# Kernel tuning notes

Measured on AMD Instinct MI355X. Metric: run time of the kernel, lower is better.

Reference implementation:

```python
import jax, jax.numpy as jnp
import numpy as np

N_V, M, K, C, H, F, CO = 100000, 25000, 48, 64, 4, 256, 64


def setup_inputs() -> dict:
    key = jax.random.key(0)
    ks = jax.random.split(key, 16)
    w = lambda k, shape: (jax.random.normal(k, shape, jnp.float32) * 0.05)
    voxel_features = jax.random.normal(ks[0], (N_V, C), jnp.float32)
    voxel_coords = jax.random.uniform(ks[1], (N_V, 3), jnp.float32) * 70.0 - 35.0
    query_coords = jax.random.uniform(ks[2], (M, 3), jnp.float32) * 70.0 - 35.0
    key_indices = jax.random.randint(ks[3], (M, K), 0, N_V, jnp.int32)
    key_mask = jax.random.uniform(ks[4], (M, K)) < 0.3
    key_mask = key_mask.at[:, 0].set(False)  # guarantee >=1 valid key per query
    zeros = lambda n: jnp.zeros((n,), jnp.float32)
    ones = lambda n: jnp.ones((n,), jnp.float32)
    return dict(
        voxel_features=voxel_features, voxel_coords=voxel_coords,
        query_coords=query_coords, key_indices=key_indices, key_mask=key_mask,
        q_pos_w=w(ks[5], (C, 3)), q_pos_b=zeros(C),
        k_pos_w=w(ks[6], (C, 3)), k_pos_b=zeros(C),
        in_proj_w=w(ks[7], (3 * C, C)), in_proj_b=zeros(3 * C),
        out_proj_w=w(ks[8], (C, C)), out_proj_b=zeros(C),
        lin1_w=w(ks[9], (F, C)), lin1_b=zeros(F),
        lin2_w=w(ks[10], (C, F)), lin2_b=zeros(C),
        norm_g=ones(C), norm_b=zeros(C), norm_m=zeros(C), norm_v=ones(C),
        out_w=w(ks[11], (CO, C)), out_b=zeros(CO),
        bn2_g=ones(CO), bn2_b=zeros(CO), bn2_m=zeros(CO), bn2_v=ones(CO),
    )


def reference(voxel_features, voxel_coords, query_coords, key_indices, key_mask,
              q_pos_w, q_pos_b, k_pos_w, k_pos_b, in_proj_w, in_proj_b,
              out_proj_w, out_proj_b, lin1_w, lin1_b, lin2_w, lin2_b,
              norm_g, norm_b, norm_m, norm_v, out_w, out_b,
              bn2_g, bn2_b, bn2_m, bn2_v):
    m, k = key_indices.shape
    c = voxel_features.shape[1]
    h = H
    d = c // h
    # grouping_operation: gather per-query key features/coords  (M,K,C)/(M,K,3)
    key_feats = voxel_features[key_indices]
    rel = voxel_coords[key_indices] - query_coords[:, None, :]  # relative coords
    # k_pos_proj: Conv1d(3->C, kernel 1) + ReLU == pointwise linear
    key_pos = jax.nn.relu(jnp.einsum('mkt,ct->mkc', rel, k_pos_w) + k_pos_b)
    k_in = key_feats + key_pos                      # (M,K,C)
    # q_pos_proj: Linear(3->C) + ReLU
    q_in = jax.nn.relu(query_coords @ q_pos_w.T + q_pos_b)  # (M,C)
    # nn.MultiheadAttention, query len 1, batch = M, keys = K
    wq, wk, wv = jnp.split(in_proj_w, 3, axis=0)
    bq, bk, bv = jnp.split(in_proj_b, 3)
    q = ((q_in @ wq.T + bq) * (d ** -0.5)).reshape(m, h, d)
    kk = (k_in @ wk.T + bk).reshape(m, k, h, d)
    vv = (k_in @ wv.T + bv).reshape(m, k, h, d)
    s = jnp.einsum('mhd,mkhd->mhk', q, kk)
    s = jnp.where(key_mask[:, None, :], -1e9, s)    # key_padding_mask
    a = jax.nn.softmax(s, axis=-1)
    o = jnp.einsum('mhk,mkhd->mhd', a, vv).reshape(m, c)
    attend = o @ out_proj_w.T + out_proj_b          # (M,C)
    # FFN residual (dropouts are identity in eval)
    ff = jax.nn.relu(attend @ lin1_w.T + lin1_b) @ lin2_w.T + lin2_b
    x = attend + ff
    # BatchNorm1d (eval)
    x = (x - norm_m) / jnp.sqrt(norm_v + 1e-5) * norm_g + norm_b
    # output_layer: Linear -> BN -> ReLU
    y = x @ out_w.T + out_b
    y = (y - bn2_m) / jnp.sqrt(bn2_v + 1e-5) * bn2_g + bn2_b
    return jax.nn.relu(y)
```

## Files before the change

kernel.cpp:

```cpp
#include <hip/hip_runtime.h>
#include <math.h>

#define CC 64
#define KK 48
#define HH 4

typedef __attribute__((ext_vector_type(8))) short s16x8;
typedef __attribute__((ext_vector_type(4))) short s16x4;
typedef __attribute__((ext_vector_type(4))) float f32x4;

#define QW_OFF_U16 57344
#define CASTB 1024

#define WAVEFENCE() asm volatile("s_waitcnt lgkmcnt(0)" ::: "memory")

__device__ __forceinline__ unsigned short f2bf(float f) {
  return (unsigned short)((__float_as_uint(f) + 0x8000u) >> 16);
}
__device__ __forceinline__ float bf2f(unsigned short h) {
  return __uint_as_float(((unsigned)h) << 16);
}

__global__ __launch_bounds__(256) void setup_kernel(
    const float* __restrict__ ipw, const float* __restrict__ opw,
    const float* __restrict__ l1w, const float* __restrict__ l2w,
    const float* __restrict__ ow,
    const float* __restrict__ ng, const float* __restrict__ nb,
    const float* __restrict__ nm, const float* __restrict__ nv,
    const float* __restrict__ b2g, const float* __restrict__ b2b,
    const float* __restrict__ b2m, const float* __restrict__ b2v,
    const unsigned char* __restrict__ km,
    const float* __restrict__ vf, const float* __restrict__ vcoord,
    const float* __restrict__ qcoord, const float* __restrict__ qpw,
    const float* __restrict__ qpb, const float* __restrict__ ipb,
    float* __restrict__ ws,
    unsigned short* __restrict__ vfb, float4* __restrict__ vc4,
    unsigned short* __restrict__ qw_out, int M, int NV)
{
  unsigned short* wsu = (unsigned short*)ws;
  const int b = blockIdx.x;

  if (b < 210) {
    if (b == 209) {
      int any = 0;
      for (int i = threadIdx.x; i < 4096; i += 256)
        if ((i & 3) && km[i]) any = 1;
      __shared__ int sb;
      if (threadIdx.x == 0) sb = 0;
      __syncthreads();
      if (any) atomicOr(&sb, 1);
      __syncthreads();
      if (threadIdx.x == 0) ((int*)ws)[26880] = sb;
      return;
    }
    int e = b * 256 + threadIdx.x;
    if (e < 4096)        wsu[e] = f2bf(ipw[e]);
    else if (e < 8192)  { int i = e - 4096; int h = i >> 10, c = (i >> 4) & 63, d = i & 15;
                          wsu[e] = f2bf(ipw[(size_t)(64 + h * 16 + d) * 64 + c]); }
    else if (e < 12288)  wsu[e] = f2bf(ipw[e]);
    else if (e < 16384)  wsu[e] = f2bf(opw[e - 12288]);
    else if (e < 32768)  wsu[e] = f2bf(l1w[e - 16384]);
    else if (e < 49152)  wsu[e] = f2bf(l2w[e - 32768]);
    else if (e < 53248)  wsu[e] = f2bf(ow[e - 49152]);
    else if (e < 53312) { int c = e - 53248; float s = ng[c] / sqrtf(nv[c] + 1e-5f);
                          ws[26624 + c] = s; ws[26624 + 64 + c] = nb[c] - nm[c] * s; }
    else if (e < 53376) { int c = e - 53312; float s = b2g[c] / sqrtf(b2v[c] + 1e-5f);
                          ws[26752 + c] = s; ws[26752 + 64 + c] = b2b[c] - b2m[c] * s; }
    return;
  }

  if (b < 210 + CASTB) {
    const int i0 = (b - 210) * 256 + threadIdx.x;
    const int stride = CASTB * 256;
    for (int i = i0; i < NV * 16; i += stride) {
      const float4 v = *(const float4*)(vf + (size_t)i * 4);
      s16x4 p; p[0] = (short)f2bf(v.x); p[1] = (short)f2bf(v.y);
      p[2] = (short)f2bf(v.z); p[3] = (short)f2bf(v.w);
      *(s16x4*)(vfb + (size_t)i * 4) = p;
    }
    for (int i = i0; i < NV; i += stride)
      vc4[i] = make_float4(vcoord[i * 3], vcoord[i * 3 + 1], vcoord[i * 3 + 2], 0.f);
    return;
  }

  {
    __shared__ __align__(16) unsigned short wql[4096];
    __shared__ __align__(16) unsigned short wkTl[4096];
    __shared__ __align__(16) unsigned short xa[4][1024];
    __shared__ float qc[4][48];
    const int w = threadIdx.x >> 6, l = threadIdx.x & 63;
    const int col = l & 15, lg = l >> 4;
    const int r0 = (b - 210 - CASTB) * 64 + w * 16;

    for (int i = threadIdx.x; i < 4096; i += 256) {
      const int r = i >> 6, d = i & 63;
      wql[i ^ ((r & 7) << 3)] = f2bf(ipw[i]);
      wkTl[(d * 64 + r) ^ ((d & 7) << 3)] = f2bf(ipw[4096 + i]);
    }
    if (l < 48) {
      int gi = r0 * 3 + l;
      qc[w][l] = (gi < M * 3) ? qcoord[gi] : 0.f;
    }
    const int c0 = col * 4;
    const float4 wA = *(const float4*)(qpw + c0 * 3);
    const float4 wB = *(const float4*)(qpw + c0 * 3 + 4);
    const float4 wC = *(const float4*)(qpw + c0 * 3 + 8);
    const float4 bq4 = *(const float4*)(qpb + c0);
    __syncthreads();

    #pragma unroll
    for (int i = 0; i < 4; ++i) {
      const int row = i * 4 + lg;
      const float x = qc[w][row * 3 + 0], y = qc[w][row * 3 + 1], z = qc[w][row * 3 + 2];
      s16x4 p;
      p[0] = (short)f2bf(fmaxf(wA.x * x + wA.y * y + wA.z * z + bq4.x, 0.f));
      p[1] = (short)f2bf(fmaxf(wA.w * x + wB.x * y + wB.y * z + bq4.y, 0.f));
      p[2] = (short)f2bf(fmaxf(wB.z * x + wB.w * y + wC.x * z + bq4.z, 0.f));
      p[3] = (short)f2bf(fmaxf(wC.y * x + wC.z * y + wC.w * z + bq4.w, 0.f));
      *(s16x4*)&xa[w][(row * 64 + c0) ^ ((row & 7) << 3)] = p;
    }
    __syncthreads();

    {
      s16x8 af0 = *(const s16x8*)&xa[w][(col * 64 + 0 + lg * 8) ^ ((col & 7) << 3)];
      s16x8 af1 = *(const s16x8*)&xa[w][(col * 64 + 32 + lg * 8) ^ ((col & 7) << 3)];
      f32x4 qv[4];
      #pragma unroll
      for (int nt = 0; nt < 4; ++nt) {
        const int n = nt * 16 + col;
        f32x4 acc = {0.f, 0.f, 0.f, 0.f};
        acc = __builtin_amdgcn_mfma_f32_16x16x32_bf16(af0,
                *(const s16x8*)&wql[(n * 64 + 0 + lg * 8) ^ ((col & 7) << 3)], acc, 0, 0, 0);
        acc = __builtin_amdgcn_mfma_f32_16x16x32_bf16(af1,
                *(const s16x8*)&wql[(n * 64 + 32 + lg * 8) ^ ((col & 7) << 3)], acc, 0, 0, 0);
        qv[nt] = acc;
      }
      __syncthreads();
      #pragma unroll
      for (int nt = 0; nt < 4; ++nt) {
        const int n = nt * 16 + col;
        const float bb = ipb[n];
        #pragma unroll
        for (int r = 0; r < 4; ++r) {
          const int row = lg * 4 + r;
          xa[w][(row * 64 + n) ^ ((row & 7) << 3)] = f2bf((qv[nt][r] + bb) * 0.25f);
        }
      }
    }
    __syncthreads();

    #pragma unroll
    for (int h = 0; h < HH; ++h) {
      s16x8 a = {0, 0, 0, 0, 0, 0, 0, 0};
      if (lg < 2)
        a = *(const s16x8*)&xa[w][(col * 64 + h * 16 + lg * 8) ^ ((col & 7) << 3)];
      #pragma unroll
      for (int nt = 0; nt < 4; ++nt) {
        const int n = nt * 16 + col;
        s16x8 bf = {0, 0, 0, 0, 0, 0, 0, 0};
        if (lg < 2)
          bf = *(const s16x8*)&wkTl[(n * 64 + h * 16 + lg * 8) ^ ((col & 7) << 3)];
        f32x4 acc = {0.f, 0.f, 0.f, 0.f};
        acc = __builtin_amdgcn_mfma_f32_16x16x32_bf16(a, bf, acc, 0, 0, 0);
        #pragma unroll
        for (int r = 0; r < 4; ++r) {
          const int m = lg * 4 + r;
          if (r0 + m < M)
            qw_out[(size_t)(r0 + m) * 256 + h * 64 + n] = f2bf(acc[r]);
        }
      }
    }
  }
}

__global__ __launch_bounds__(256, 4) void attn_hot(
    const unsigned short* __restrict__ vfb, const float4* __restrict__ vc4,
    const float* __restrict__ qcoord, const int* __restrict__ kidx,
    const unsigned char* __restrict__ km8, const int* __restrict__ km32,
    const int* __restrict__ maskfmt,
    const float* __restrict__ kpw, const float* __restrict__ kpb,
    const float* __restrict__ ipb,
    const unsigned short* __restrict__ wv_bf,
    const unsigned short* __restrict__ qw_pre,
    float* __restrict__ out, int M)
{
  __shared__ __align__(16) unsigned short shq[4][3456];
  const int w = threadIdx.x >> 6, l = threadIdx.x & 63;
  const int col = l & 15, lg = l >> 4;
  int m = blockIdx.x * 4 + w;
  if (m >= M) m = M - 1;
  unsigned short* sh = shq[w];
  float* relf = (float*)(sh + 3072);
  const int is_u8 = *maskfmt;

  s16x8 wvb[4][2];
  #pragma unroll
  for (int nt = 0; nt < 4; ++nt)
    #pragma unroll
    for (int kst = 0; kst < 2; ++kst)
      wvb[nt][kst] = *(const s16x8*)(wv_bf + (size_t)(nt * 16 + col) * 64 + kst * 32 + lg * 8);

  const float qx = qcoord[m * 3 + 0], qy = qcoord[m * 3 + 1], qz = qcoord[m * 3 + 2];
  const int c0 = col * 4;
  const float4 kwA = *(const float4*)(kpw + c0 * 3);
  const float4 kwB = *(const float4*)(kpw + c0 * 3 + 4);
  const float4 kwC = *(const float4*)(kpw + c0 * 3 + 8);
  const float4 kbv = *(const float4*)(kpb + c0);

  const s16x8 qb0 = *(const s16x8*)(qw_pre + (size_t)m * 256 + (col & 3) * 64 + 0 + lg * 8);
  const s16x8 qb1 = *(const s16x8*)(qw_pre + (size_t)m * 256 + (col & 3) * 64 + 32 + lg * 8);

  unsigned char msk = 0;
  if (l < KK) {
    const int idx = kidx[m * KK + l];
    msk = is_u8 ? km8[m * KK + l] : (unsigned char)(km32[m * KK + l] != 0);
    const float4 vc = vc4[idx];
    float4 rr;
    rr.x = vc.x - qx; rr.y = vc.y - qy; rr.z = vc.z - qz;
    rr.w = __int_as_float(idx);
    *(float4*)(relf + l * 4) = rr;
  }
  const unsigned long long bm = __ballot(l < KK && msk);
  WAVEFENCE();

  #pragma unroll
  for (int half = 0; half < 2; ++half) {
    float4 ra[6]; s16x4 va[6];
    #pragma unroll
    for (int j = 0; j < 6; ++j) {
      const int k = half * 24 + j * 4 + lg;
      ra[j] = *(const float4*)(relf + k * 4);
      va[j] = *(const s16x4*)(vfb + (size_t)__float_as_int(ra[j].w) * 64 + c0);
    }
    #pragma unroll
    for (int j = 0; j < 6; ++j) {
      const int k = half * 24 + j * 4 + lg;
      const float p0 = fmaxf(kwA.x * ra[j].x + kwA.y * ra[j].y + kwA.z * ra[j].z + kbv.x, 0.f);
      const float p1 = fmaxf(kwA.w * ra[j].x + kwB.x * ra[j].y + kwB.y * ra[j].z + kbv.y, 0.f);
      const float p2 = fmaxf(kwB.z * ra[j].x + kwB.w * ra[j].y + kwC.x * ra[j].z + kbv.z, 0.f);
      const float p3 = fmaxf(kwC.y * ra[j].x + kwC.z * ra[j].y + kwC.w * ra[j].z + kbv.w, 0.f);
      s16x4 p;
      p[0] = (short)f2bf(bf2f((unsigned short)va[j][0]) + p0);
      p[1] = (short)f2bf(bf2f((unsigned short)va[j][1]) + p1);
      p[2] = (short)f2bf(bf2f((unsigned short)va[j][2]) + p2);
      p[3] = (short)f2bf(bf2f((unsigned short)va[j][3]) + p3);
      *(s16x4*)&sh[(k * 64 + c0) ^ ((k & 7) << 3)] = p;
    }
  }
  WAVEFENCE();

  s16x8 af[3][2];
  #pragma unroll
  for (int mt = 0; mt < 3; ++mt)
    #pragma unroll
    for (int kst = 0; kst < 2; ++kst) {
      const int row = mt * 16 + col;
      af[mt][kst] = *(const s16x8*)&sh[(row * 64 + kst * 32 + lg * 8) ^ ((row & 7) << 3)];
    }
  f32x4 sc[3];
  sc[0] = sc[1] = sc[2] = (f32x4){0.f, 0.f, 0.f, 0.f};
  __builtin_amdgcn_s_setprio(1);
  #pragma unroll
  for (int mt = 0; mt < 3; ++mt) {
    sc[mt] = __builtin_amdgcn_mfma_f32_16x16x32_bf16(af[mt][0], qb0, sc[mt], 0, 0, 0);
    sc[mt] = __builtin_amdgcn_mfma_f32_16x16x32_bf16(af[mt][1], qb1, sc[mt], 0, 0, 0);
  }
  __builtin_amdgcn_s_setprio(0);

  float sv[12];
  {
    float mx = -INFINITY;
    #pragma unroll
    for (int mt = 0; mt < 3; ++mt)
      #pragma unroll
      for (int r = 0; r < 4; ++r) {
        const int key = mt * 16 + lg * 4 + r;
        float v = sc[mt][r];
        if ((bm >> key) & 1ull) v = -1e30f;
        sv[mt * 4 + r] = v;
        mx = fmaxf(mx, v);
      }
    mx = fmaxf(mx, __shfl_xor(mx, 16, 64));
    mx = fmaxf(mx, __shfl_xor(mx, 32, 64));
    float sum = 0.f;
    #pragma unroll
    for (int i = 0; i < 12; ++i) { float e = __expf(sv[i] - mx); sv[i] = e; sum += e; }
    sum += __shfl_xor(sum, 16, 64);
    sum += __shfl_xor(sum, 32, 64);
    const float inv = 1.f / sum;
    #pragma unroll
    for (int i = 0; i < 12; ++i) sv[i] *= inv;
  }
  if (col < HH) {
    #pragma unroll
    for (int mt = 0; mt < 3; ++mt)
      #pragma unroll
      for (int r = 0; r < 4; ++r)
        relf[(mt * 16 + lg * 4 + r) * 4 + col] = sv[mt * 4 + r];
  }
  WAVEFENCE();

  f32x4 vva[4][3];
  __builtin_amdgcn_s_setprio(1);
  #pragma unroll
  for (int nt = 0; nt < 4; ++nt) {
    vva[nt][0] = vva[nt][1] = vva[nt][2] = (f32x4){0.f, 0.f, 0.f, 0.f};
    #pragma unroll
    for (int kst = 0; kst < 2; ++kst) {
      vva[nt][0] = __builtin_amdgcn_mfma_f32_16x16x32_bf16(af[0][kst], wvb[nt][kst], vva[nt][0], 0, 0, 0);
      vva[nt][1] = __builtin_amdgcn_mfma_f32_16x16x32_bf16(af[1][kst], wvb[nt][kst], vva[nt][1], 0, 0, 0);
      vva[nt][2] = __builtin_amdgcn_mfma_f32_16x16x32_bf16(af[2][kst], wvb[nt][kst], vva[nt][2], 0, 0, 0);
    }
  }
  __builtin_amdgcn_s_setprio(0);
  float op[4] = {0.f, 0.f, 0.f, 0.f};
  #pragma unroll
  for (int mt = 0; mt < 3; ++mt)
    #pragma unroll
    for (int r = 0; r < 4; ++r) {
      const float4 a4 = *(const float4*)(relf + (mt * 16 + lg * 4 + r) * 4);
      op[0] += a4.x * vva[0][mt][r];
      op[1] += a4.y * vva[1][mt][r];
      op[2] += a4.z * vva[2][mt][r];
      op[3] += a4.w * vva[3][mt][r];
    }
  #pragma unroll
  for (int nt = 0; nt < 4; ++nt) {
    op[nt] += __shfl_xor(op[nt], 16, 64);
    op[nt] += __shfl_xor(op[nt], 32, 64);
  }
  {
    float oo = (lg == 0) ? op[0] : (lg == 1) ? op[1] : (lg == 2) ? op[2] : op[3];
    oo += ipb[2 * CC + lg * 16 + col];
    out[(size_t)m * CC + lg * 16 + col] = oo;
  }
}

__global__ __launch_bounds__(256) void prep_kernel(
    const float* __restrict__ ipw, const float* __restrict__ opw,
    const float* __restrict__ l1w, const float* __restrict__ l2w,
    const float* __restrict__ ow,
    const float* __restrict__ ng, const float* __restrict__ nb,
    const float* __restrict__ nm, const float* __restrict__ nv,
    const float* __restrict__ b2g, const float* __restrict__ b2b,
    const float* __restrict__ b2m, const float* __restrict__ b2v,
    const unsigned char* __restrict__ km,
    float* __restrict__ ws)
{
  unsigned short* wsu = (unsigned short*)ws;
  if (blockIdx.x == 209) {
    int any = 0;
    for (int i = threadIdx.x; i < 4096; i += 256)
      if ((i & 3) && km[i]) any = 1;
    __shared__ int sb;
    if (threadIdx.x == 0) sb = 0;
    __syncthreads();
    if (any) atomicOr(&sb, 1);
    __syncthreads();
    if (threadIdx.x == 0) ((int*)ws)[26880] = sb;
    return;
  }
  int e = blockIdx.x * 256 + threadIdx.x;
  if (e < 4096)        wsu[e] = f2bf(ipw[e]);
  else if (e < 8192)  { int i = e - 4096; int h = i >> 10, c = (i >> 4) & 63, d = i & 15;
                        wsu[e] = f2bf(ipw[(size_t)(64 + h * 16 + d) * 64 + c]); }
  else if (e < 12288)  wsu[e] = f2bf(ipw[e]);
  else if (e < 16384)  wsu[e] = f2bf(opw[e - 12288]);
  else if (e < 32768)  wsu[e] = f2bf(l1w[e - 16384]);
  else if (e < 49152)  wsu[e] = f2bf(l2w[e - 32768]);
  else if (e < 53248)  wsu[e] = f2bf(ow[e - 49152]);
  else if (e < 53312) { int c = e - 53248; float s = ng[c] / sqrtf(nv[c] + 1e-5f);
                        ws[26624 + c] = s; ws[26624 + 64 + c] = nb[c] - nm[c] * s; }
  else if (e < 53376) { int c = e - 53312; float s = b2g[c] / sqrtf(b2v[c] + 1e-5f);
                        ws[26752 + c] = s; ws[26752 + 64 + c] = b2b[c] - b2m[c] * s; }
}

__global__ __launch_bounds__(256, 4) void attn_fallback(
    const float* __restrict__ vfeat, const float* __restrict__ vcoord,
    const float* __restrict__ qcoord, const int* __restrict__ kidx,
    const unsigned char* __restrict__ km8, const int* __restrict__ km32,
    const int* __restrict__ maskfmt,
    const float* __restrict__ qpw, const float* __restrict__ qpb,
    const float* __restrict__ kpw, const float* __restrict__ kpb,
    const float* __restrict__ ipb,
    const unsigned short* __restrict__ wq_bf,
    const unsigned short* __restrict__ wk2T_bf,
    const unsigned short* __restrict__ wv_bf,
    float* __restrict__ out, int M)
{
  __shared__ __align__(16) unsigned short shq[4][3776];
  __shared__ __align__(16) unsigned short wvl[4096];
  const int w = threadIdx.x >> 6, l = threadIdx.x & 63;
  const int col = l & 15, lg = l >> 4;
  int m = blockIdx.x * 4 + w;
  if (m >= M) m = M - 1;
  unsigned short* sh = shq[w];
  const int is_u8 = *maskfmt;
  float* relf = (float*)sh + 1696;

  #pragma unroll
  for (int i = 0; i < 2; ++i) {
    const int ch = threadIdx.x * 2 + i;
    const int n = ch >> 3, g = ch & 7;
    const s16x8 v = *(const s16x8*)(wv_bf + n * 64 + g * 8);
    *(s16x8*)&wvl[n * 64 + ((g ^ (n & 7)) << 3)] = v;
  }

  const float qx = qcoord[m * 3 + 0], qy = qcoord[m * 3 + 1], qz = qcoord[m * 3 + 2];
  const int c0 = col * 4;
  const float4 kwA = *(const float4*)(kpw + c0 * 3);
  const float4 kwB = *(const float4*)(kpw + c0 * 3 + 4);
  const float4 kwC = *(const float4*)(kpw + c0 * 3 + 8);
  const float4 kbv = *(const float4*)(kpb + c0);

  {
    float v = qpw[l * 3 + 0] * qx + qpw[l * 3 + 1] * qy + qpw[l * 3 + 2] * qz + qpb[l];
    sh[3328 + l] = f2bf(fmaxf(v, 0.f));
  }
  unsigned char msk = 0;
  if (l < KK) {
    int idx = kidx[m * KK + l];
    msk = is_u8 ? km8[m * KK + l] : (unsigned char)(km32[m * KK + l] != 0);
    relf[l * 4 + 0] = vcoord[idx * 3 + 0] - qx;
    relf[l * 4 + 1] = vcoord[idx * 3 + 1] - qy;
    relf[l * 4 + 2] = vcoord[idx * 3 + 2] - qz;
    relf[l * 4 + 3] = __int_as_float(idx);
  }
  const unsigned long long bm = __ballot(l < KK && msk);
  __syncthreads();

  {
    f32x4 qacc[4];
    #pragma unroll
    for (int nt = 0; nt < 4; ++nt) qacc[nt] = (f32x4){0.f, 0.f, 0.f, 0.f};
    #pragma unroll
    for (int kst = 0; kst < 2; ++kst) {
      const s16x8 a = *(const s16x8*)&sh[3328 + kst * 32 + lg * 8];
      #pragma unroll
      for (int nt = 0; nt < 4; ++nt) {
        const s16x8 b = *(const s16x8*)(wq_bf + (nt * 16 + col) * 64 + kst * 32 + lg * 8);
        qacc[nt] = __builtin_amdgcn_mfma_f32_16x16x32_bf16(a, b, qacc[nt], 0, 0, 0);
      }
    }
    __syncthreads();
    if (lg == 0) {
      #pragma unroll
      for (int nt = 0; nt < 4; ++nt)
        sh[3328 + nt * 16 + col] = f2bf((qacc[nt][0] + ipb[nt * 16 + col]) * 0.25f);
    }
    __syncthreads();
    f32x4 wacc[4];
    #pragma unroll
    for (int nt = 0; nt < 4; ++nt) wacc[nt] = (f32x4){0.f, 0.f, 0.f, 0.f};
    #pragma unroll
    for (int kst = 0; kst < 2; ++kst) {
      const int hblk = kst * 2 + (lg >> 1);
      s16x8 a = {0, 0, 0, 0, 0, 0, 0, 0};
      if (col == hblk) a = *(const s16x8*)&sh[3328 + kst * 32 + lg * 8];
      #pragma unroll
      for (int nt = 0; nt < 4; ++nt) {
        const s16x8 b = *(const s16x8*)(wk2T_bf + hblk * 1024 + (nt * 16 + col) * 16 + (lg & 1) * 8);
        wacc[nt] = __builtin_amdgcn_mfma_f32_16x16x32_bf16(a, b, wacc[nt], 0, 0, 0);
      }
    }
    if (lg == 0) {
      #pragma unroll
      for (int nt = 0; nt < 4; ++nt)
        #pragma unroll
        for (int r = 0; r < 4; ++r)
          sh[3072 + r * 64 + nt * 16 + col] = f2bf(wacc[nt][r]);
    }
  }

  #pragma unroll
  for (int half = 0; half < 2; ++half) {
    float4 ra[6], va[6];
    #pragma unroll
    for (int j = 0; j < 6; ++j) {
      const int k = half * 24 + j * 4 + lg;
      ra[j] = *(const float4*)(relf + k * 4);
      va[j] = *(const float4*)(vfeat + (size_t)__float_as_int(ra[j].w) * 64 + c0);
    }
    #pragma unroll
    for (int j = 0; j < 6; ++j) {
      const int k = half * 24 + j * 4 + lg;
      const float p0 = fmaxf(kwA.x * ra[j].x + kwA.y * ra[j].y + kwA.z * ra[j].z + kbv.x, 0.f);
      const float p1 = fmaxf(kwA.w * ra[j].x + kwB.x * ra[j].y + kwB.y * ra[j].z + kbv.y, 0.f);
      const float p2 = fmaxf(kwB.z * ra[j].x + kwB.w * ra[j].y + kwC.x * ra[j].z + kbv.z, 0.f);
      const float p3 = fmaxf(kwC.y * ra[j].x + kwC.z * ra[j].y + kwC.w * ra[j].z + kbv.w, 0.f);
      s16x4 p;
      p[0] = (short)f2bf(va[j].x + p0); p[1] = (short)f2bf(va[j].y + p1);
      p[2] = (short)f2bf(va[j].z + p2); p[3] = (short)f2bf(va[j].w + p3);
      *(s16x4*)&sh[(k * 64 + c0) ^ ((k & 7) << 3)] = p;
    }
  }
  __syncthreads();

  s16x8 af[3][2];
  #pragma unroll
  for (int mt = 0; mt < 3; ++mt)
    #pragma unroll
    for (int kst = 0; kst < 2; ++kst) {
      const int row = mt * 16 + col;
      af[mt][kst] = *(const s16x8*)&sh[(row * 64 + kst * 32 + lg * 8) ^ ((row & 7) << 3)];
    }
  f32x4 sc[3];
  sc[0] = sc[1] = sc[2] = (f32x4){0.f, 0.f, 0.f, 0.f};
  #pragma unroll
  for (int kst = 0; kst < 2; ++kst) {
    const s16x8 b = *(const s16x8*)&sh[3072 + (col & 3) * 64 + kst * 32 + lg * 8];
    #pragma unroll
    for (int mt = 0; mt < 3; ++mt)
      sc[mt] = __builtin_amdgcn_mfma_f32_16x16x32_bf16(af[mt][kst], b, sc[mt], 0, 0, 0);
  }

  float sv[12];
  {
    float mx = -INFINITY;
    #pragma unroll
    for (int mt = 0; mt < 3; ++mt)
      #pragma unroll
      for (int r = 0; r < 4; ++r) {
        const int key = mt * 16 + lg * 4 + r;
        float v = sc[mt][r];
        if ((bm >> key) & 1ull) v = -1e30f;
        sv[mt * 4 + r] = v;
        mx = fmaxf(mx, v);
      }
    mx = fmaxf(mx, __shfl_xor(mx, 16, 64));
    mx = fmaxf(mx, __shfl_xor(mx, 32, 64));
    float sum = 0.f;
    #pragma unroll
    for (int i = 0; i < 12; ++i) { float e = __expf(sv[i] - mx); sv[i] = e; sum += e; }
    sum += __shfl_xor(sum, 16, 64);
    sum += __shfl_xor(sum, 32, 64);
    const float inv = 1.f / sum;
    #pragma unroll
    for (int i = 0; i < 12; ++i) sv[i] *= inv;
  }

  float op[4];
  #pragma unroll
  for (int nt = 0; nt < 4; ++nt) {
    const int n = nt * 16 + col;
    f32x4 vv0 = {0.f, 0.f, 0.f, 0.f}, vv1 = vv0, vv2 = vv0;
    #pragma unroll
    for (int kst = 0; kst < 2; ++kst) {
      const s16x8 b = *(const s16x8*)&wvl[(n * 64 + kst * 32 + lg * 8) ^ ((n & 7) << 3)];
      vv0 = __builtin_amdgcn_mfma_f32_16x16x32_bf16(af[0][kst], b, vv0, 0, 0, 0);
      vv1 = __builtin_amdgcn_mfma_f32_16x16x32_bf16(af[1][kst], b, vv1, 0, 0, 0);
      vv2 = __builtin_amdgcn_mfma_f32_16x16x32_bf16(af[2][kst], b, vv2, 0, 0, 0);
    }
    const int src = lg * 16 + nt;
    float o = 0.f;
    #pragma unroll
    for (int mt = 0; mt < 3; ++mt)
      #pragma unroll
      for (int r = 0; r < 4; ++r) {
        const float a = __shfl(sv[mt * 4 + r], src, 64);
        const float v = (mt == 0) ? vv0[r] : (mt == 1) ? vv1[r] : vv2[r];
        o += a * v;
      }
    op[nt] = o;
  }
  #pragma unroll
  for (int nt = 0; nt < 4; ++nt) {
    op[nt] += __shfl_xor(op[nt], 16, 64);
    op[nt] += __shfl_xor(op[nt], 32, 64);
  }
  {
    float oo = (lg == 0) ? op[0] : (lg == 1) ? op[1] : (lg == 2) ? op[2] : op[3];
    oo += ipb[2 * CC + lg * 16 + col];
    out[(size_t)m * CC + lg * 16 + col] = oo;
  }
}

__global__ __launch_bounds__(256, 2) void chain_kernel(
    float* __restrict__ inout, const unsigned short* __restrict__ wsu,
    const float* __restrict__ opb, const float* __restrict__ l1b,
    const float* __restrict__ l2b, const float* __restrict__ ob,
    const float* __restrict__ nrm, const float* __restrict__ bn2, int M)
{
  __shared__ short lds[4][5120];
  const int w = threadIdx.x >> 6;
  const int l = threadIdx.x & 63;
  const int col = l & 15, lg = l >> 4;
  const int r0 = blockIdx.x * 64 + w * 16;

  short* XH = &lds[w][0];
  short* XB = &lds[w][4096];
  const unsigned short* opw_bf = wsu + 12288;
  const unsigned short* l1_bf  = wsu + 16384;
  const unsigned short* l2_bf  = wsu + 32768;
  const unsigned short* ow_bf  = wsu + 49152;

  #pragma unroll
  for (int i = 0; i < 4; ++i) {
    int row = i * 4 + lg, cb = col * 4;
    float4 v = make_float4(0.f, 0.f, 0.f, 0.f);
    if (r0 + row < M) v = *(const float4*)(&inout[(size_t)(r0 + row) * 64 + cb]);
    s16x4 p; p[0] = (short)f2bf(v.x); p[1] = (short)f2bf(v.y);
    p[2] = (short)f2bf(v.z); p[3] = (short)f2bf(v.w);
    *(s16x4*)&XH[(row * 64 + cb) ^ ((row & 7) << 3)] = p;
  }

  s16x8 afa[2];
  #pragma unroll
  for (int kst = 0; kst < 2; ++kst)
    afa[kst] = *(const s16x8*)&XH[(col * 64 + kst * 32 + lg * 8) ^ ((col & 7) << 3)];
  f32x4 att[4];
  #pragma unroll
  for (int nt = 0; nt < 4; ++nt) {
    f32x4 acc = {0.f, 0.f, 0.f, 0.f};
    #pragma unroll
    for (int kst = 0; kst < 2; ++kst) {
      const s16x8 b = *(const s16x8*)&opw_bf[(nt * 16 + col) * 64 + kst * 32 + lg * 8];
      acc = __builtin_amdgcn_mfma_f32_16x16x32_bf16(afa[kst], b, acc, 0, 0, 0);
    }
    float bias = opb[nt * 16 + col];
    #pragma unroll
    for (int r = 0; r < 4; ++r) {
      acc[r] += bias;
      int row = lg * 4 + r;
      XB[(row * 64 + nt * 16 + col) ^ ((row & 7) << 3)] = (short)f2bf(acc[r]);
    }
    att[nt] = acc;
  }

  s16x8 afb[2];
  #pragma unroll
  for (int kst = 0; kst < 2; ++kst)
    afb[kst] = *(const s16x8*)&XB[(col * 64 + kst * 32 + lg * 8) ^ ((col & 7) << 3)];
  #pragma unroll
  for (int nt = 0; nt < 16; ++nt) {
    f32x4 acc = {0.f, 0.f, 0.f, 0.f};
    #pragma unroll
    for (int kst = 0; kst < 2; ++kst) {
      const s16x8 b = *(const s16x8*)&l1_bf[(nt * 16 + col) * 64 + kst * 32 + lg * 8];
      acc = __builtin_amdgcn_mfma_f32_16x16x32_bf16(afb[kst], b, acc, 0, 0, 0);
    }
    float bias = l1b[nt * 16 + col];
    #pragma unroll
    for (int r = 0; r < 4; ++r) {
      float h = fmaxf(acc[r] + bias, 0.f);
      int row = lg * 4 + r;
      XH[(row * 256 + nt * 16 + col) ^ ((row & 7) << 3)] = (short)f2bf(h);
    }
  }

  s16x8 afh[8];
  #pragma unroll
  for (int kst = 0; kst < 8; ++kst)
    afh[kst] = *(const s16x8*)&XH[(col * 256 + kst * 32 + lg * 8) ^ ((col & 7) << 3)];
  #pragma unroll
  for (int nt = 0; nt < 4; ++nt) {
    f32x4 acc = {0.f, 0.f, 0.f, 0.f};
    #pragma unroll
    for (int kst = 0; kst < 8; ++kst) {
      const s16x8 b = *(const s16x8*)&l2_bf[(nt * 16 + col) * 256 + kst * 32 + lg * 8];
      acc = __builtin_amdgcn_mfma_f32_16x16x32_bf16(afh[kst], b, acc, 0, 0, 0);
    }
    int nc = nt * 16 + col;
    float bias = l2b[nc], sN = nrm[nc], tN = nrm[64 + nc];
    #pragma unroll
    for (int r = 0; r < 4; ++r) {
      float x = (att[nt][r] + acc[r] + bias) * sN + tN;
      int row = lg * 4 + r;
      XB[(row * 64 + nc) ^ ((row & 7) << 3)] = (short)f2bf(x);
    }
  }

  s16x8 afx[2];
  #pragma unroll
  for (int kst = 0; kst < 2; ++kst)
    afx[kst] = *(const s16x8*)&XB[(col * 64 + kst * 32 + lg * 8) ^ ((col & 7) << 3)];
  #pragma unroll
  for (int nt = 0; nt < 4; ++nt) {
    f32x4 acc = {0.f, 0.f, 0.f, 0.f};
    #pragma unroll
    for (int kst = 0; kst < 2; ++kst) {
      const s16x8 b = *(const s16x8*)&ow_bf[(nt * 16 + col) * 64 + kst * 32 + lg * 8];
      acc = __builtin_amdgcn_mfma_f32_16x16x32_bf16(afx[kst], b, acc, 0, 0, 0);
    }
    int nc = nt * 16 + col;
    float bias = ob[nc], sB = bn2[nc], tB = bn2[64 + nc];
    #pragma unroll
    for (int r = 0; r < 4; ++r) {
      float y = fmaxf((acc[r] + bias) * sB + tB, 0.f);
      int row = lg * 4 + r;
      if (r0 + row < M) inout[(size_t)(r0 + row) * 64 + nc] = y;
    }
  }
}

extern "C" void kernel_launch(void* const* d_in, const int* in_sizes, int n_in,
                              void* d_out, int out_size, void* d_ws, size_t ws_size,
                              hipStream_t stream) {
  const float* vfeat  = (const float*)d_in[0];
  const float* vcoord = (const float*)d_in[1];
  const float* qcoord = (const float*)d_in[2];
  const int*   kidx   = (const int*)d_in[3];
  const unsigned char* km8  = (const unsigned char*)d_in[4];
  const int*           km32 = (const int*)d_in[4];
  const float* qpw = (const float*)d_in[5];
  const float* qpb = (const float*)d_in[6];
  const float* kpw = (const float*)d_in[7];
  const float* kpb = (const float*)d_in[8];
  const float* ipw = (const float*)d_in[9];
  const float* ipb = (const float*)d_in[10];
  const float* opw = (const float*)d_in[11];
  const float* opb = (const float*)d_in[12];
  const float* l1w = (const float*)d_in[13];
  const float* l1b = (const float*)d_in[14];
  const float* l2w = (const float*)d_in[15];
  const float* l2b = (const float*)d_in[16];
  const float* ng  = (const float*)d_in[17];
  const float* nb  = (const float*)d_in[18];
  const float* nm  = (const float*)d_in[19];
  const float* nv  = (const float*)d_in[20];
  const float* ow  = (const float*)d_in[21];
  const float* ob  = (const float*)d_in[22];
  const float* b2g = (const float*)d_in[23];
  const float* b2b = (const float*)d_in[24];
  const float* b2m = (const float*)d_in[25];
  const float* b2v = (const float*)d_in[26];

  const int M  = in_sizes[2] / 3;
  const int NV = in_sizes[0] / 64;
  float* ws  = (float*)d_ws;
  float* out = (float*)d_out;
  unsigned short* wsu = (unsigned short*)ws;
  const int* flag = (const int*)ws + 26880;

  const size_t need = (size_t)114688 + (size_t)M * 512 + (size_t)NV * 128 + (size_t)NV * 16;
  const int hot = (ws_size >= need) ? 1 : 0;
  unsigned short* qw  = wsu + QW_OFF_U16;
  unsigned short* vfb = wsu + QW_OFF_U16 + (size_t)M * 256;
  float4* vc4 = (float4*)(wsu + QW_OFF_U16 + (size_t)M * 256 + (size_t)NV * 64);

  if (hot) {
    const int qblocks = (M + 63) / 64;
    setup_kernel<<<210 + CASTB + qblocks, 256, 0, stream>>>(
        ipw, opw, l1w, l2w, ow, ng, nb, nm, nv, b2g, b2b, b2m, b2v, km8,
        vfeat, vcoord, qcoord, qpw, qpb, ipb, ws, vfb, vc4, qw, M, NV);
    attn_hot<<<(M + 3) / 4, 256, 0, stream>>>(vfb, vc4, qcoord, kidx,
                                              km8, km32, flag, kpw, kpb, ipb,
                                              wsu + 8192, qw, out, M);
  } else {
    prep_kernel<<<210, 256, 0, stream>>>(ipw, opw, l1w, l2w, ow,
                                         ng, nb, nm, nv, b2g, b2b, b2m, b2v, km8, ws);
    attn_fallback<<<(M + 3) / 4, 256, 0, stream>>>(vfeat, vcoord, qcoord, kidx,
                                                   km8, km32, flag,
                                                   qpw, qpb, kpw, kpb, ipb,
                                                   wsu, wsu + 4096, wsu + 8192, out, M);
  }
  chain_kernel<<<(M + 63) / 64, 256, 0, stream>>>(out, wsu, opb, l1b, l2b, ob,
                                                  ws + 26624, ws + 26752, M);
}
```

Measured before the change: 95.91 us.

## Split FFN chain across waves per 16-row tile and stage Wv in LDS

The post-attention chain kernel now gives each 256-thread block 16 rows instead of 64. Its four waves split the output columns of each GEMM and exchange activations through shared LDS with block barriers, which launches four times as many blocks with less per-wave register and LDS pressure. The attention kernel also loads the Wv bf16 weights cooperatively into a swizzled LDS buffer instead of holding eight weight vectors per lane in registers, with the wave fence replaced by a block barrier. The intent is higher occupancy and lower register use. The cost is extra block-wide syncs, more redundant weight fetches per row, and LDS reads on the MFMA path.

```diff
diff --git a/kernel.cpp b/kernel.cpp
--- a/kernel.cpp
+++ b/kernel.cpp
@@ -185,6 +185,7 @@
     float* __restrict__ out, int M)
 {
   __shared__ __align__(16) unsigned short shq[4][3456];
+  __shared__ __align__(16) unsigned short wvl[4096];
   const int w = threadIdx.x >> 6, l = threadIdx.x & 63;
   const int col = l & 15, lg = l >> 4;
   int m = blockIdx.x * 4 + w;
@@ -193,12 +194,13 @@
   float* relf = (float*)(sh + 3072);
   const int is_u8 = *maskfmt;
 
-  s16x8 wvb[4][2];
-  #pragma unroll
-  for (int nt = 0; nt < 4; ++nt)
-    #pragma unroll
-    for (int kst = 0; kst < 2; ++kst)
-      wvb[nt][kst] = *(const s16x8*)(wv_bf + (size_t)(nt * 16 + col) * 64 + kst * 32 + lg * 8);
+  #pragma unroll
+  for (int i = 0; i < 2; ++i) {
+    const int ch = threadIdx.x * 2 + i;
+    const int n = ch >> 3, g = ch & 7;
+    const s16x8 v = *(const s16x8*)(wv_bf + n * 64 + g * 8);
+    *(s16x8*)&wvl[n * 64 + ((g ^ (n & 7)) << 3)] = v;
+  }
 
   const float qx = qcoord[m * 3 + 0], qy = qcoord[m * 3 + 1], qz = qcoord[m * 3 + 2];
   const int c0 = col * 4;
@@ -221,7 +223,7 @@
     *(float4*)(relf + l * 4) = rr;
   }
   const unsigned long long bm = __ballot(l < KK && msk);
-  WAVEFENCE();
+  __syncthreads();
 
   #pragma unroll
   for (int half = 0; half < 2; ++half) {
@@ -304,12 +306,14 @@
   __builtin_amdgcn_s_setprio(1);
   #pragma unroll
   for (int nt = 0; nt < 4; ++nt) {
+    const int n = nt * 16 + col;
     vva[nt][0] = vva[nt][1] = vva[nt][2] = (f32x4){0.f, 0.f, 0.f, 0.f};
     #pragma unroll
     for (int kst = 0; kst < 2; ++kst) {
-      vva[nt][0] = __builtin_amdgcn_mfma_f32_16x16x32_bf16(af[0][kst], wvb[nt][kst], vva[nt][0], 0, 0, 0);
-      vva[nt][1] = __builtin_amdgcn_mfma_f32_16x16x32_bf16(af[1][kst], wvb[nt][kst], vva[nt][1], 0, 0, 0);
-      vva[nt][2] = __builtin_amdgcn_mfma_f32_16x16x32_bf16(af[2][kst], wvb[nt][kst], vva[nt][2], 0, 0, 0);
+      const s16x8 bb = *(const s16x8*)&wvl[(n * 64 + kst * 32 + lg * 8) ^ ((n & 7) << 3)];
+      vva[nt][0] = __builtin_amdgcn_mfma_f32_16x16x32_bf16(af[0][kst], bb, vva[nt][0], 0, 0, 0);
+      vva[nt][1] = __builtin_amdgcn_mfma_f32_16x16x32_bf16(af[1][kst], bb, vva[nt][1], 0, 0, 0);
+      vva[nt][2] = __builtin_amdgcn_mfma_f32_16x16x32_bf16(af[2][kst], bb, vva[nt][2], 0, 0, 0);
     }
   }
   __builtin_amdgcn_s_setprio(0);
@@ -333,6 +337,128 @@
     float oo = (lg == 0) ? op[0] : (lg == 1) ? op[1] : (lg == 2) ? op[2] : op[3];
     oo += ipb[2 * CC + lg * 16 + col];
     out[(size_t)m * CC + lg * 16 + col] = oo;
+  }
+}
+
+__global__ __launch_bounds__(256, 4) void chain2_kernel(
+    float* __restrict__ inout, const unsigned short* __restrict__ wsu,
+    const float* __restrict__ opb, const float* __restrict__ l1b,
+    const float* __restrict__ l2b, const float* __restrict__ ob,
+    const float* __restrict__ nrm, const float* __restrict__ bn2, int M)
+{
+  __shared__ __align__(16) unsigned short XA[1024];
+  __shared__ __align__(16) unsigned short XH[4096];
+  __shared__ __align__(16) unsigned short XB[1024];
+  const int w = threadIdx.x >> 6, l = threadIdx.x & 63;
+  const int col = l & 15, lg = l >> 4;
+  const int r0 = blockIdx.x * 16;
+
+  const unsigned short* opw_bf = wsu + 12288;
+  const unsigned short* l1_bf  = wsu + 16384;
+  const unsigned short* l2_bf  = wsu + 32768;
+  const unsigned short* ow_bf  = wsu + 49152;
+
+  {
+    const int i = threadIdx.x;
+    const int row = i >> 4, cb = (i & 15) * 4;
+    float4 v = make_float4(0.f, 0.f, 0.f, 0.f);
+    if (r0 + row < M) v = *(const float4*)(&inout[(size_t)(r0 + row) * 64 + cb]);
+    s16x4 p; p[0] = (short)f2bf(v.x); p[1] = (short)f2bf(v.y);
+    p[2] = (short)f2bf(v.z); p[3] = (short)f2bf(v.w);
+    *(s16x4*)&XA[(row * 64 + cb) ^ ((row & 7) << 3)] = p;
+  }
+  __syncthreads();
+
+  s16x8 afa[2];
+  #pragma unroll
+  for (int kst = 0; kst < 2; ++kst)
+    afa[kst] = *(const s16x8*)&XA[(col * 64 + kst * 32 + lg * 8) ^ ((col & 7) << 3)];
+  f32x4 att;
+  {
+    f32x4 acc = {0.f, 0.f, 0.f, 0.f};
+    #pragma unroll
+    for (int kst = 0; kst < 2; ++kst) {
+      const s16x8 bb = *(const s16x8*)&opw_bf[(w * 16 + col) * 64 + kst * 32 + lg * 8];
+      acc = __builtin_amdgcn_mfma_f32_16x16x32_bf16(afa[kst], bb, acc, 0, 0, 0);
+    }
+    const float bias = opb[w * 16 + col];
+    #pragma unroll
+    for (int r = 0; r < 4; ++r) {
+      acc[r] += bias;
+      const int row = lg * 4 + r;
+      XB[(row * 64 + w * 16 + col) ^ ((row & 7) << 3)] = (short)f2bf(acc[r]);
+    }
+    att = acc;
+  }
+  __syncthreads();
+
+  {
+    s16x8 afb[2];
+    #pragma unroll
+    for (int kst = 0; kst < 2; ++kst)
+      afb[kst] = *(const s16x8*)&XB[(col * 64 + kst * 32 + lg * 8) ^ ((col & 7) << 3)];
+    #pragma unroll
+    for (int nt2 = 0; nt2 < 4; ++nt2) {
+      const int ntg = w * 4 + nt2;
+      f32x4 acc = {0.f, 0.f, 0.f, 0.f};
+      #pragma unroll
+      for (int kst = 0; kst < 2; ++kst) {
+        const s16x8 bb = *(const s16x8*)&l1_bf[(ntg * 16 + col) * 64 + kst * 32 + lg * 8];
+        acc = __builtin_amdgcn_mfma_f32_16x16x32_bf16(afb[kst], bb, acc, 0, 0, 0);
+      }
+      const float bias = l1b[ntg * 16 + col];
+      #pragma unroll
+      for (int r = 0; r < 4; ++r) {
+        const float h = fmaxf(acc[r] + bias, 0.f);
+        const int row = lg * 4 + r;
+        XH[(row * 256 + ntg * 16 + col) ^ ((row & 7) << 3)] = (short)f2bf(h);
+      }
+    }
+  }
+  __syncthreads();
+
+  {
+    s16x8 afh[8];
+    #pragma unroll
+    for (int kst = 0; kst < 8; ++kst)
+      afh[kst] = *(const s16x8*)&XH[(col * 256 + kst * 32 + lg * 8) ^ ((col & 7) << 3)];
+    f32x4 acc = {0.f, 0.f, 0.f, 0.f};
+    #pragma unroll
+    for (int kst = 0; kst < 8; ++kst) {
+      const s16x8 bb = *(const s16x8*)&l2_bf[(w * 16 + col) * 256 + kst * 32 + lg * 8];
+      acc = __builtin_amdgcn_mfma_f32_16x16x32_bf16(afh[kst], bb, acc, 0, 0, 0);
+    }
+    const int nc = w * 16 + col;
+    const float bias = l2b[nc], sN = nrm[nc], tN = nrm[64 + nc];
+    __syncthreads();
+    #pragma unroll
+    for (int r = 0; r < 4; ++r) {
+      const float x = (att[r] + acc[r] + bias) * sN + tN;
+      const int row = lg * 4 + r;
+      XB[(row * 64 + nc) ^ ((row & 7) << 3)] = (short)f2bf(x);
+    }
+  }
+  __syncthreads();
+
+  {
+    s16x8 afx[2];
+    #pragma unroll
+    for (int kst = 0; kst < 2; ++kst)
+      afx[kst] = *(const s16x8*)&XB[(col * 64 + kst * 32 + lg * 8) ^ ((col & 7) << 3)];
+    f32x4 acc = {0.f, 0.f, 0.f, 0.f};
+    #pragma unroll
+    for (int kst = 0; kst < 2; ++kst) {
+      const s16x8 bb = *(const s16x8*)&ow_bf[(w * 16 + col) * 64 + kst * 32 + lg * 8];
+      acc = __builtin_amdgcn_mfma_f32_16x16x32_bf16(afx[kst], bb, acc, 0, 0, 0);
+    }
+    const int nc = w * 16 + col;
+    const float bias = ob[nc], sB = bn2[nc], tB = bn2[64 + nc];
+    #pragma unroll
+    for (int r = 0; r < 4; ++r) {
+      const float y = fmaxf((acc[r] + bias) * sB + tB, 0.f);
+      const int q = r0 + lg * 4 + r;
+      if (q < M) inout[(size_t)q * 64 + nc] = y;
+    }
   }
 }
 
@@ -572,124 +698,6 @@
     float oo = (lg == 0) ? op[0] : (lg == 1) ? op[1] : (lg == 2) ? op[2] : op[3];
     oo += ipb[2 * CC + lg * 16 + col];
     out[(size_t)m * CC + lg * 16 + col] = oo;
-  }
-}
-
-__global__ __launch_bounds__(256, 2) void chain_kernel(
-    float* __restrict__ inout, const unsigned short* __restrict__ wsu,
-    const float* __restrict__ opb, const float* __restrict__ l1b,
-    const float* __restrict__ l2b, const float* __restrict__ ob,
-    const float* __restrict__ nrm, const float* __restrict__ bn2, int M)
-{
-  __shared__ short lds[4][5120];
-  const int w = threadIdx.x >> 6;
-  const int l = threadIdx.x & 63;
-  const int col = l & 15, lg = l >> 4;
-  const int r0 = blockIdx.x * 64 + w * 16;
-
-  short* XH = &lds[w][0];
-  short* XB = &lds[w][4096];
-  const unsigned short* opw_bf = wsu + 12288;
-  const unsigned short* l1_bf  = wsu + 16384;
-  const unsigned short* l2_bf  = wsu + 32768;
-  const unsigned short* ow_bf  = wsu + 49152;
-
-  #pragma unroll
-  for (int i = 0; i < 4; ++i) {
-    int row = i * 4 + lg, cb = col * 4;
-    float4 v = make_float4(0.f, 0.f, 0.f, 0.f);
-    if (r0 + row < M) v = *(const float4*)(&inout[(size_t)(r0 + row) * 64 + cb]);
-    s16x4 p; p[0] = (short)f2bf(v.x); p[1] = (short)f2bf(v.y);
-    p[2] = (short)f2bf(v.z); p[3] = (short)f2bf(v.w);
-    *(s16x4*)&XH[(row * 64 + cb) ^ ((row & 7) << 3)] = p;
-  }
-
-  s16x8 afa[2];
-  #pragma unroll
-  for (int kst = 0; kst < 2; ++kst)
-    afa[kst] = *(const s16x8*)&XH[(col * 64 + kst * 32 + lg * 8) ^ ((col & 7) << 3)];
-  f32x4 att[4];
-  #pragma unroll
-  for (int nt = 0; nt < 4; ++nt) {
-    f32x4 acc = {0.f, 0.f, 0.f, 0.f};
-    #pragma unroll
-    for (int kst = 0; kst < 2; ++kst) {
-      const s16x8 b = *(const s16x8*)&opw_bf[(nt * 16 + col) * 64 + kst * 32 + lg * 8];
-      acc = __builtin_amdgcn_mfma_f32_16x16x32_bf16(afa[kst], b, acc, 0, 0, 0);
-    }
-    float bias = opb[nt * 16 + col];
-    #pragma unroll
-    for (int r = 0; r < 4; ++r) {
-      acc[r] += bias;
-      int row = lg * 4 + r;
-      XB[(row * 64 + nt * 16 + col) ^ ((row & 7) << 3)] = (short)f2bf(acc[r]);
-    }
-    att[nt] = acc;
-  }
-
-  s16x8 afb[2];
-  #pragma unroll
-  for (int kst = 0; kst < 2; ++kst)
-    afb[kst] = *(const s16x8*)&XB[(col * 64 + kst * 32 + lg * 8) ^ ((col & 7) << 3)];
-  #pragma unroll
-  for (int nt = 0; nt < 16; ++nt) {
-    f32x4 acc = {0.f, 0.f, 0.f, 0.f};
-    #pragma unroll
-    for (int kst = 0; kst < 2; ++kst) {
-      const s16x8 b = *(const s16x8*)&l1_bf[(nt * 16 + col) * 64 + kst * 32 + lg * 8];
-      acc = __builtin_amdgcn_mfma_f32_16x16x32_bf16(afb[kst], b, acc, 0, 0, 0);
-    }
-    float bias = l1b[nt * 16 + col];
-    #pragma unroll
-    for (int r = 0; r < 4; ++r) {
-      float h = fmaxf(acc[r] + bias, 0.f);
-      int row = lg * 4 + r;
-      XH[(row * 256 + nt * 16 + col) ^ ((row & 7) << 3)] = (short)f2bf(h);
-    }
-  }
-
-  s16x8 afh[8];
-  #pragma unroll
-  for (int kst = 0; kst < 8; ++kst)
-    afh[kst] = *(const s16x8*)&XH[(col * 256 + kst * 32 + lg * 8) ^ ((col & 7) << 3)];
-  #pragma unroll
-  for (int nt = 0; nt < 4; ++nt) {
-    f32x4 acc = {0.f, 0.f, 0.f, 0.f};
-    #pragma unroll
-    for (int kst = 0; kst < 8; ++kst) {
-      const s16x8 b = *(const s16x8*)&l2_bf[(nt * 16 + col) * 256 + kst * 32 + lg * 8];
-      acc = __builtin_amdgcn_mfma_f32_16x16x32_bf16(afh[kst], b, acc, 0, 0, 0);
-    }
-    int nc = nt * 16 + col;
-    float bias = l2b[nc], sN = nrm[nc], tN = nrm[64 + nc];
-    #pragma unroll
-    for (int r = 0; r < 4; ++r) {
-      float x = (att[nt][r] + acc[r] + bias) * sN + tN;
-      int row = lg * 4 + r;
-      XB[(row * 64 + nc) ^ ((row & 7) << 3)] = (short)f2bf(x);
-    }
-  }
-
-  s16x8 afx[2];
-  #pragma unroll
-  for (int kst = 0; kst < 2; ++kst)
-    afx[kst] = *(const s16x8*)&XB[(col * 64 + kst * 32 + lg * 8) ^ ((col & 7) << 3)];
-  #pragma unroll
-  for (int nt = 0; nt < 4; ++nt) {
-    f32x4 acc = {0.f, 0.f, 0.f, 0.f};
-    #pragma unroll
-    for (int kst = 0; kst < 2; ++kst) {
-      const s16x8 b = *(const s16x8*)&ow_bf[(nt * 16 + col) * 64 + kst * 32 + lg * 8];
-      acc = __builtin_amdgcn_mfma_f32_16x16x32_bf16(afx[kst], b, acc, 0, 0, 0);
-    }
-    int nc = nt * 16 + col;
-    float bias = ob[nc], sB = bn2[nc], tB = bn2[64 + nc];
-    #pragma unroll
-    for (int r = 0; r < 4; ++r) {
-      float y = fmaxf((acc[r] + bias) * sB + tB, 0.f);
-      int row = lg * 4 + r;
-      if (r0 + row < M) inout[(size_t)(r0 + row) * 64 + nc] = y;
-    }
   }
 }
 
@@ -754,6 +762,6 @@
                                                    qpw, qpb, kpw, kpb, ipb,
                                                    wsu, wsu + 4096, wsu + 8192, out, M);
   }
-  chain_kernel<<<(M + 63) / 64, 256, 0, stream>>>(out, wsu, opb, l1b, l2b, ob,
-                                                  ws + 26624, ws + 26752, M);
+  chain2_kernel<<<(M + 15) / 16, 256, 0, stream>>>(out, wsu, opb, l1b, l2b, ob,
+                                                   ws + 26624, ws + 26752, M);
 }
```

Measured after the change: 80.61 us. 16.0% less time.
